# Optimization experiments

Hardware: AMD Instinct MI355X
Metric: run time of the kernel (lower is better)

Reference implementation:

```python
import jax, jax.numpy as jnp
import numpy as np

L = 48                 # lattice side
M = 2 * L * L          # 4608 spin-orbitals (spinful: 2 per site)
N_OCC = 1024           # occupied fermions
N_HID = 24             # hidden fermions
NT2 = 2 * N_HID        # pairing channels in CNN output
JASTROW = 16
CH = NT2 + JASTROW     # 64 CNN channels
NBLOCKS = 4
K = 3                  # conv kernel size


def conv2d_circular(x, w, b):
    # x: (C,H,W), w: (O,I,K,K); 'SAME' conv with circular (periodic) padding
    p = K // 2
    xp = jnp.pad(x, ((0, 0), (p, p), (p, p)), mode='wrap')
    y = jax.lax.conv_general_dilated(xp[None], w, (1, 1), 'VALID',
                                     dimension_numbers=('NCHW', 'OIHW', 'NCHW'))[0]
    if b is not None:
        y = y + b[:, None, None]
    return y


def cnn_forward(x, params):
    # ReshapeConv: flat spinful config (M,) -> (2, L, L)
    h = x.reshape(2, L, L)
    for i, (w1, b1, w2, b2) in enumerate(params):
        res = h
        t = h / jnp.sqrt(i + 1.0)
        t = t / jnp.sqrt(2.0) if i == 0 else jax.nn.gelu(t)
        t = jax.nn.gelu(conv2d_circular(t, w1, b1))
        t = conv2d_circular(t, w2, b2)
        if t.shape[0] > res.shape[0]:
            res = jnp.repeat(res, t.shape[0] // res.shape[0], axis=0)
        h = t + res
    return h / jnp.sqrt(NBLOCKS + 1.0)


def pfaffian_sign(A):
    # Sign of the Pfaffian of skew-symmetric A via Householder tridiagonalization.
    # pf(A) = det(Q) * prod(superdiag of T over even positions); det(Q)=(-1)^{#reflections}.
    n = A.shape[0]
    idx = jnp.arange(n)

    def body(k, carry):
        A, ds = carry
        col = A[:, k]
        xv = jnp.where(idx > k, col, 0.0)
        normx = jnp.sqrt(jnp.sum(xv * xv))
        s = jnp.where(col[k + 1] >= 0, 1.0, -1.0)
        v = xv - (-s * normx) * (idx == k + 1).astype(A.dtype)
        vn = jnp.sqrt(jnp.sum(v * v))
        ok = vn > 1e-30
        v = jnp.where(ok, v / jnp.where(ok, vn, 1.0), 0.0)
        u = A @ v
        # H A H for skew A with H = I - 2 v v^T  (v^T A v = 0)
        A = A + 2.0 * jnp.outer(v, u) - 2.0 * jnp.outer(u, v)
        return A, jnp.where(ok, -ds, ds)

    A, ds = jax.lax.fori_loop(0, n - 2, body, (A, jnp.array(1.0, A.dtype)))
    sup = jnp.diagonal(A, offset=1)[::2]
    return ds * jnp.prod(jnp.sign(sup))


def setup_inputs() -> dict:
    key = jax.random.key(0)
    ks = jax.random.split(key, 32)
    # occupation config in {+1,-1} with exactly N_OCC occupied modes
    occ = jnp.concatenate([jnp.ones(N_OCC, jnp.float32), -jnp.ones(M - N_OCC, jnp.float32)])
    x = jax.random.permutation(ks[0], occ)

    def he(k, shape):
        fan_in = shape[1] * shape[2] * shape[3]
        return jax.random.normal(k, shape, jnp.float32) * jnp.sqrt(2.0 / fan_in)

    inp = {
        'x': x,
        'F_vv': jax.random.normal(ks[1], (M, M), jnp.float32),
        'F_hh': jax.random.normal(ks[2], (N_HID, N_HID), jnp.float32),
    }
    j = 3
    for b in range(NBLOCKS):
        cin = 2 if b == 0 else CH
        inp[f'w1_{b}'] = he(ks[j], (CH, cin, K, K)); j += 1
        inp[f'b1_{b}'] = jnp.zeros((CH,), jnp.float32)
        inp[f'w2_{b}'] = he(ks[j], (CH, CH, K, K)); j += 1
        if b < NBLOCKS - 1:  # last block conv2 has no bias
            inp[f'b2_{b}'] = jnp.zeros((CH,), jnp.float32)
    return inp


def reference(x, F_vv, F_hh,
              w1_0, b1_0, w2_0, b2_0,
              w1_1, b1_1, w2_1, b2_1,
              w1_2, b1_2, w2_2, b2_2,
              w1_3, b1_3, w2_3):
    params = [(w1_0, b1_0, w2_0, b2_0),
              (w1_1, b1_1, w2_1, b2_1),
              (w1_2, b1_2, w2_2, b2_2),
              (w1_3, b1_3, w2_3, None)]
    out = cnn_forward(x, params)                     # (CH, L, L)
    n = jnp.nonzero(x == 1, size=N_OCC)[0]           # occupied mode indices
    log_J = out[NT2:].sum()                          # Jastrow log-factor (real)
    F_vh = out[:NT2].reshape(-1, M).T                # (M, N_HID)
    Fvv = 0.5 * (F_vv - F_vv.T)
    Fvh_n = F_vh[n]                                  # (N_OCC, N_HID)
    A = jnp.block([[Fvv[n][:, n], Fvh_n],
                   [-Fvh_n.T, 0.5 * (F_hh - F_hh.T)]])  # (N_OCC+N_HID,)^2 skew
    sign = pfaffian_sign(jax.lax.stop_gradient(A))   # cos(angle(sign)) == sign for real dtype
    logabspf = 0.5 * jnp.linalg.slogdet(A)[1]        # |pf(A)| = sqrt(|det(A)|)
    return sign, logabspf + log_J
```

## Files before the change

### kernel.cpp

```cpp
#include <hip/hip_runtime.h>
#include <math.h>


#define NPIX 2304
#define MSZ  4608
#define NOCC 1024
#define NHID 24
#define PF_N 1048

__device__ __forceinline__ float gelu_f(float v){
  float v3 = v*v*v;
  return 0.5f*v*(1.0f + tanhf(0.7978845608028654f*(v + 0.044715f*v3)));
}

__global__ void k_prep(const float* __restrict__ x, int* __restrict__ nidx,
                       float* __restrict__ tbuf){
  __shared__ int cnt[256];
  __shared__ int off[256];
  int t = threadIdx.x;
  int c = 0;
  for (int k = 0; k < 18; k++){
    int idx = t*18 + k;
    float v = x[idx];
    c += (v == 1.0f) ? 1 : 0;
    tbuf[idx] = v * 0.70710678118654752f;
  }
  cnt[t] = c;
  __syncthreads();
  if (t == 0){ int s = 0; for (int q=0;q<256;q++){ off[q]=s; s+=cnt[q]; } }
  __syncthreads();
  int o = off[t];
  for (int k = 0; k < 18; k++){
    int idx = t*18+k;
    if (x[idx] == 1.0f) nidx[o++] = idx;
  }
}

__global__ __launch_bounds__(128) void k_conv(const float* __restrict__ in,
      const float* __restrict__ wgt, const float* __restrict__ bias,
      const float* __restrict__ res, float* __restrict__ outp,
      float* __restrict__ pre_out, double* __restrict__ logJ_acc,
      int cin, int resmode, int dogelu, float scale, float pre_scale){
  const int c  = blockIdx.x / 6;
  const int rg = blockIdx.x % 6;
  const int tid = threadIdx.x;
  const int y  = rg*8 + (tid >> 4);
  const int xg = (tid & 15)*3;
  const int ym = ((y+47)%48)*48, y0 = y*48, yp = ((y+1)%48)*48;
  int c5[5];
  #pragma unroll
  for (int t = 0; t < 5; t++){
    int xx = xg - 1 + t;
    c5[t] = (xx < 0) ? 47 : ((xx >= 48) ? xx - 48 : xx);
  }
  float s0 = 0.f, s1 = 0.f, s2 = 0.f;
  const float* wp = wgt + c*cin*9;
  for (int ci = 0; ci < cin; ci++){
    const float* b_ = in + ci*NPIX;
    #pragma unroll
    for (int rr = 0; rr < 3; rr++){
      const int rb = (rr == 0) ? ym : ((rr == 1) ? y0 : yp);
      float v0 = b_[rb+c5[0]], v1 = b_[rb+c5[1]], v2 = b_[rb+c5[2]];
      float v3 = b_[rb+c5[3]], v4 = b_[rb+c5[4]];
      float w0 = wp[3*rr], w1 = wp[3*rr+1], w2 = wp[3*rr+2];
      s0 += v0*w0 + v1*w1 + v2*w2;
      s1 += v1*w0 + v2*w1 + v3*w2;
      s2 += v2*w0 + v3*w1 + v4*w2;
    }
    wp += 9;
  }
  const float bv = bias ? bias[c] : 0.f;
  const int base = c*NPIX + y0 + xg;
  float sv[3] = {s0, s1, s2};
  double ls = 0.0;
  #pragma unroll
  for (int t = 0; t < 3; t++){
    float s = sv[t] + bv;
    if (dogelu) s = gelu_f(s);
    if (resmode == 1) s += res[c*NPIX + y0 + xg + t];
    else if (resmode == 2) s += res[(c>>5)*NPIX + y0 + xg + t];
    s *= scale;
    outp[base+t] = s;
    if (pre_out) pre_out[base+t] = gelu_f(s * pre_scale);
    ls += (double)s;
  }
  if (logJ_acc && c >= 48){
    for (int o = 32; o > 0; o >>= 1) ls += __shfl_down(ls, o, 64);
    if ((tid & 63) == 0) atomicAdd(logJ_acc, ls);
  }
}

__global__ __launch_bounds__(256) void k_buildAvv(const float* __restrict__ Fvv,
      const int* __restrict__ nidx, double* __restrict__ A){
  __shared__ float G1[32][33], G2[32][33];
  __shared__ int sNi[32], sNj[32];
  int I = 0, item = blockIdx.x;
  while ((I+1)*(I+2)/2 <= item) I++;
  const int J = item - I*(I+1)/2;
  const int i0 = I*32, j0 = J*32;
  const int tid = threadIdx.x;
  if (tid < 32){ sNi[tid] = nidx[i0+tid]; }
  else if (tid < 64){ sNj[tid-32] = nidx[j0+tid-32]; }
  __syncthreads();
  for (int idx = tid; idx < 32*32; idx += 256){
    const int r = idx >> 5, c = idx & 31;
    G1[r][c] = Fvv[(size_t)sNi[r]*MSZ + sNj[c]];
    G2[r][c] = Fvv[(size_t)sNj[r]*MSZ + sNi[c]];
  }
  __syncthreads();
  for (int idx = tid; idx < 32*32; idx += 256){
    const int r = idx >> 5, c = idx & 31;
    const int i = i0 + r, j = j0 + c;
    if (i > j)
      A[(size_t)i*PF_N + j] = 0.5*((double)G1[r][c] - (double)G2[c][r]);
  }
}

__global__ void k_buildAs(const float* __restrict__ Fhh,
      const float* __restrict__ hfin, const int* __restrict__ nidx,
      double* __restrict__ A){
  int g = blockIdx.x*256 + threadIdx.x;
  if (g >= 24*PF_N) return;
  const int i = NOCC + g / PF_N, j = g % PF_N;
  if (j >= i) return;
  const int r = i - NOCC;
  double v;
  if (j < NOCC){
    int nj = nidx[j];
    int ss = (nj >= NPIX) ? 1 : 0;
    v = -(double)hfin[(2*r+ss)*NPIX + (nj - ss*NPIX)];
  } else {
    int r2 = j - NOCC;
    v = 0.5*((double)Fhh[r*NHID + r2] - (double)Fhh[r2*NHID + r]);
  }
  A[(size_t)i*PF_N + j] = v;
}

__device__ __forceinline__ void factor_lds(double* D, double* sTf, int w,
      double* __restrict__ histN, double& lv_out, int& sg_out){
  const int tid = threadIdx.x;
  const int r = tid & 63, qu = tid >> 6;
  const int np = w >> 1;
  for (int j = 0; j < np; j++){
    const int r0 = 2*j, r1 = r0 + 1;
    const double t = -D[r1*65 + r0];
    const double invt = 1.0 / t;
    if (tid == 0) sTf[j] = t;
    const bool rowok = (r < w) && (r >= r0 + 2);
    if (rowok){
      const double ar = D[r*65 + r0], br = D[r*65 + r1];
      if (qu == 0){
        histN[32 + j*64 + r]        = ar * invt;
        histN[32 + 2048 + j*64 + r] = br * invt;
      }
      const int lo = r0 + 2, hi = r;
      const int per = (hi - lo + 3) >> 2;
      const int cb = lo + qu*per;
      int ce = cb + per; if (ce > hi) ce = hi;
      for (int c = cb; c < ce; c++){
        const double ac = D[c*65 + r0], bc = D[c*65 + r1];
        D[r*65 + c] += (br*ac - ar*bc) * invt;
      }
    }
    __syncthreads();
  }
  if (tid < np) histN[tid] = 1.0 / sTf[tid];
  lv_out = 0.0; sg_out = 0;
  if (tid < 64){
    double lv = 0.0; int sg = 0;
    if (tid < np){ double t = sTf[tid]; lv = log(fabs(t)); sg = (t < 0.0) ? 1 : 0; }
    for (int o = 32; o > 0; o >>= 1){
      lv += __shfl_down(lv, o, 64);
      sg += __shfl_down(sg, o, 64);
    }
    if (tid == 0){ lv_out = lv; sg_out = sg; }
  }
}

__global__ __launch_bounds__(256) void k_panelD0(const double* __restrict__ A,
      double* __restrict__ hist, double* __restrict__ lacc,
      int* __restrict__ nneg){
  __shared__ double D[64*65];
  __shared__ double sTf[32];
  const int tid = threadIdx.x;
  for (int idx = tid; idx < 64*64; idx += 256){
    int r = idx >> 6, c = idx & 63;
    if (r > c) D[r*65+c] = A[(size_t)r*PF_N + c];
  }
  __syncthreads();
  double lv; int sg;
  factor_lds(D, sTf, 64, hist, lv, sg);
  if (tid == 0){ atomicAdd(lacc, lv); atomicAdd(nneg, sg); }
}

__global__ __launch_bounds__(256) void k_panelR(double* __restrict__ A,
      const double* __restrict__ hist, int k){
  const int N = PF_N, c0 = 64*k, tc0 = c0 + 64;
  const int wv = threadIdx.x >> 6, lc = threadIdx.x & 63;
  const int i = tc0 + blockIdx.x*4 + wv;
  if (i >= N) return;
  double v = A[(size_t)i*N + c0 + lc];
  const double* hA = hist + 32;
  const double* hB = hist + 32 + 2048;
  #pragma unroll 8
  for (int j = 0; j < 32; j++){
    double a = __shfl(v, 2*j,   64);
    double b = __shfl(v, 2*j+1, 64);
    if (lc >= 2*j+2) v += b*hA[j*64+lc] - a*hB[j*64+lc];
  }
  A[(size_t)i*N + c0 + lc] = v;
}

__global__ __launch_bounds__(256) void k_trail(double* __restrict__ A,
      const double* __restrict__ histR, double* __restrict__ histW,
      double* __restrict__ lacc, int* __restrict__ nneg,
      const double* __restrict__ logJ, float* __restrict__ outp,
      int k, int fin){
  const int N = PF_N, c0 = 64*k, tc0 = c0 + 64;
  const int tid = threadIdx.x;
  int I = 0, item = blockIdx.x;
  while ((I+1)*(I+2)/2 <= item) I++;
  const int J = item - I*(I+1)/2;
  const int i0 = tc0 + I*64, j0 = tc0 + J*64;
  const int iend = (i0 + 64 < N) ? (i0 + 64) : N;
  const int jend = (j0 + 64 < N) ? (j0 + 64) : N;
  __shared__ double shmem[4224];
  __shared__ double sInvL[32];
  __shared__ double sTf[32];
  double* sPiA = shmem;
  double* sPiB = shmem + 1056;
  double* sPjA = shmem + 2112;
  double* sPjB = shmem + 3168;
  if (tid < 32) sInvL[tid] = histR[tid];
  const int ty = tid >> 4, tx = tid & 15;
  double acc[4][4];
  #pragma unroll
  for (int rr = 0; rr < 4; rr++)
    #pragma unroll
    for (int cc = 0; cc < 4; cc++){
      const int i = i0 + ty + 16*rr, j = j0 + tx + 16*cc;
      acc[rr][cc] = (i < iend && j < jend && i > j) ? A[(size_t)i*N + j] : 0.0;
    }
  __syncthreads();
  #pragma unroll
  for (int lh = 0; lh < 2; lh++){
    #pragma unroll
    for (int u = 0; u < 4; u++){
      const int idx = tid + u*256;
      const int r = idx >> 4, ll = idx & 15;
      const int l = lh*16 + ll;
      const double it = sInvL[l];
      const int gi = i0 + r;
      double a = 0.0, b = 0.0;
      if (gi < iend){
        a = A[(size_t)gi*N + c0 + 2*l];
        b = A[(size_t)gi*N + c0 + 2*l + 1];
      }
      sPiA[ll*66+r] = a; sPiB[ll*66+r] = b;
      const int gj = j0 + r;
      double a2 = 0.0, b2 = 0.0;
      if (gj < jend){
        a2 = A[(size_t)gj*N + c0 + 2*l];
        b2 = A[(size_t)gj*N + c0 + 2*l + 1];
      }
      sPjA[ll*66+r] = a2*it; sPjB[ll*66+r] = b2*it;
    }
    __syncthreads();
    #pragma unroll 4
    for (int ll = 0; ll < 16; ll++){
      double ar[4], br[4], ac[4], bc[4];
      #pragma unroll
      for (int rr = 0; rr < 4; rr++){
        ar[rr] = sPiA[ll*66 + ty + 16*rr];
        br[rr] = sPiB[ll*66 + ty + 16*rr];
      }
      #pragma unroll
      for (int cc = 0; cc < 4; cc++){
        ac[cc] = sPjA[ll*66 + tx + 16*cc];
        bc[cc] = sPjB[ll*66 + tx + 16*cc];
      }
      #pragma unroll
      for (int rr = 0; rr < 4; rr++)
        #pragma unroll
        for (int cc = 0; cc < 4; cc++)
          acc[rr][cc] += br[rr]*ac[cc] - ar[rr]*bc[cc];
    }
    __syncthreads();
  }
  #pragma unroll
  for (int rr = 0; rr < 4; rr++)
    #pragma unroll
    for (int cc = 0; cc < 4; cc++){
      const int i = i0 + ty + 16*rr, j = j0 + tx + 16*cc;
      if (i < iend && j < jend && i > j) A[(size_t)i*N + j] = acc[rr][cc];
    }
  if (blockIdx.x == 0){
    __syncthreads();
    const int wn = iend - i0;
    #pragma unroll
    for (int rr = 0; rr < 4; rr++)
      #pragma unroll
      for (int cc = 0; cc < 4; cc++){
        const int i = i0 + ty + 16*rr, j = j0 + tx + 16*cc;
        if (i < iend && j < jend && i > j)
          shmem[(i - i0)*65 + (j - j0)] = acc[rr][cc];
      }
    __syncthreads();
    double lv; int sg;
    factor_lds(shmem, sTf, wn, histW, lv, sg);
    if (tid == 0){
      double lold = atomicAdd(lacc, lv);
      int sold = atomicAdd(nneg, sg);
      if (fin){
        int stot = sold + sg;
        outp[0] = (stot & 1) ? -1.0f : 1.0f;
        outp[1] = (float)(lold + lv + logJ[0]);
      }
    }
  }
}

extern "C" void kernel_launch(void* const* d_in, const int* in_sizes, int n_in,
                              void* d_out, int out_size, void* d_ws, size_t ws_size,
                              hipStream_t stream){
  (void)in_sizes; (void)n_in; (void)out_size; (void)ws_size;
  const float* x   = (const float*)d_in[0];
  const float* Fvv = (const float*)d_in[1];
  const float* Fhh = (const float*)d_in[2];
  const float* w1[4] = {(const float*)d_in[3], (const float*)d_in[7],
                        (const float*)d_in[11], (const float*)d_in[15]};
  const float* b1[4] = {(const float*)d_in[4], (const float*)d_in[8],
                        (const float*)d_in[12], (const float*)d_in[16]};
  const float* w2[4] = {(const float*)d_in[5], (const float*)d_in[9],
                        (const float*)d_in[13], (const float*)d_in[17]};
  const float* b2[3] = {(const float*)d_in[6], (const float*)d_in[10],
                        (const float*)d_in[14]};

  char* ws = (char*)d_ws;
  double* lacc  = (double*)(ws + 0);
  int*    nneg  = (int*)(ws + 8);
  double* logJa = (double*)(ws + 1024);
  int*    nidx  = (int*)(ws + 1088);
  double* hist0 = (double*)(ws + 8192);
  double* hist1 = (double*)(ws + 41216);
  const size_t CB = 589824;
  float* tbuf  = (float*)(ws + 74240);
  float* ybuf  = (float*)(ws + 74240 + CB);
  float* hbuf0 = (float*)(ws + 74240 + 2*CB);
  float* hbuf1 = (float*)(ws + 74240 + 3*CB);
  double* A    = (double*)(ws + 74240 + 4*CB);

  hipMemsetAsync(d_ws, 0, 2048, stream);
  k_prep<<<1,256,0,stream>>>(x, nidx, tbuf);

  k_conv<<<384,128,0,stream>>>(tbuf, w1[0], b1[0], nullptr, ybuf,
                               nullptr, nullptr, 2, 0, 1, 1.0f, 0.f);
  k_conv<<<384,128,0,stream>>>(ybuf, w2[0], b2[0], x, hbuf0,
                               tbuf, nullptr, 64, 2, 0, 1.0f,
                               0.70710678118654752f);
  k_conv<<<384,128,0,stream>>>(tbuf, w1[1], b1[1], nullptr, ybuf,
                               nullptr, nullptr, 64, 0, 1, 1.0f, 0.f);
  k_conv<<<384,128,0,stream>>>(ybuf, w2[1], b2[1], hbuf0, hbuf1,
                               tbuf, nullptr, 64, 1, 0, 1.0f,
                               0.57735026918962576f);
  k_conv<<<384,128,0,stream>>>(tbuf, w1[2], b1[2], nullptr, ybuf,
                               nullptr, nullptr, 64, 0, 1, 1.0f, 0.f);
  k_conv<<<384,128,0,stream>>>(ybuf, w2[2], b2[2], hbuf1, hbuf0,
                               tbuf, nullptr, 64, 1, 0, 1.0f, 0.5f);
  k_conv<<<384,128,0,stream>>>(tbuf, w1[3], b1[3], nullptr, ybuf,
                               nullptr, nullptr, 64, 0, 1, 1.0f, 0.f);
  k_conv<<<384,128,0,stream>>>(ybuf, w2[3], nullptr, hbuf0, hbuf1,
                               nullptr, logJa, 64, 1, 0,
                               0.44721359549995794f, 0.f);

  k_buildAvv<<<528,256,0,stream>>>(Fvv, nidx, A);
  k_buildAs<<<(24*PF_N+255)/256,256,0,stream>>>(Fhh, hbuf1, nidx, A);

  k_panelD0<<<1,256,0,stream>>>(A, hist0, lacc, nneg);
  for (int k = 0; k < 16; k++){
    double* hR = (k & 1) ? hist1 : hist0;
    double* hW = (k & 1) ? hist0 : hist1;
    const int m = PF_N - 64*(k+1);
    k_panelR<<<(m+3)/4,256,0,stream>>>(A, hR, k);
    const int nt = (m + 63) >> 6;
    k_trail<<<nt*(nt+1)/2,256,0,stream>>>(A, hR, hW, lacc, nneg, logJa,
                                          (float*)d_out, k, (k == 15) ? 1 : 0);
  }
}
```

Before: 1.119 ms.

## Fuse whole pipeline into one cooperative persistent kernel with grid syncs

Replaces the separate prep, conv, A-build, panel and trailing-update launches with a single cooperative kernel. Stages are separated by grid-wide barriers. Fvv gather tiles and the first panel factorization now run on spare blocks while the conv layers execute. This removes per-launch overhead and idle gaps between the roughly forty small kernels. In exchange, every stage is capped at 256 resident blocks, and each grid.sync adds its own barrier cost.

```diff
diff --git a/kernel.cpp b/kernel.cpp
--- a/kernel.cpp
+++ b/kernel.cpp
@@ -1,5 +1,8 @@
 #include <hip/hip_runtime.h>
+#include <hip/hip_cooperative_groups.h>
 #include <math.h>
+
+namespace cg = cooperative_groups;
 
 
 #define NPIX 2304
@@ -13,37 +16,14 @@
   return 0.5f*v*(1.0f + tanhf(0.7978845608028654f*(v + 0.044715f*v3)));
 }
 
-__global__ void k_prep(const float* __restrict__ x, int* __restrict__ nidx,
-                       float* __restrict__ tbuf){
-  __shared__ int cnt[256];
-  __shared__ int off[256];
-  int t = threadIdx.x;
-  int c = 0;
-  for (int k = 0; k < 18; k++){
-    int idx = t*18 + k;
-    float v = x[idx];
-    c += (v == 1.0f) ? 1 : 0;
-    tbuf[idx] = v * 0.70710678118654752f;
-  }
-  cnt[t] = c;
-  __syncthreads();
-  if (t == 0){ int s = 0; for (int q=0;q<256;q++){ off[q]=s; s+=cnt[q]; } }
-  __syncthreads();
-  int o = off[t];
-  for (int k = 0; k < 18; k++){
-    int idx = t*18+k;
-    if (x[idx] == 1.0f) nidx[o++] = idx;
-  }
-}
-
-__global__ __launch_bounds__(128) void k_conv(const float* __restrict__ in,
-      const float* __restrict__ wgt, const float* __restrict__ bias,
-      const float* __restrict__ res, float* __restrict__ outp,
-      float* __restrict__ pre_out, double* __restrict__ logJ_acc,
-      int cin, int resmode, int dogelu, float scale, float pre_scale){
-  const int c  = blockIdx.x / 6;
-  const int rg = blockIdx.x % 6;
-  const int tid = threadIdx.x;
+__device__ __forceinline__ void conv_unit(int u, int tid,
+    const float* __restrict__ in, const float* __restrict__ wgt,
+    const float* __restrict__ bias, const float* __restrict__ res,
+    float* __restrict__ outp, float* __restrict__ pre_out,
+    double* __restrict__ logJ_acc,
+    int cin, int resmode, int dogelu, float scale, float pre_scale){
+  const int c  = u / 6;
+  const int rg = u % 6;
   const int y  = rg*8 + (tid >> 4);
   const int xg = (tid & 15)*3;
   const int ym = ((y+47)%48)*48, y0 = y*48, yp = ((y+1)%48)*48;
@@ -90,50 +70,30 @@
   }
 }
 
-__global__ __launch_bounds__(256) void k_buildAvv(const float* __restrict__ Fvv,
-      const int* __restrict__ nidx, double* __restrict__ A){
-  __shared__ float G1[32][33], G2[32][33];
-  __shared__ int sNi[32], sNj[32];
-  int I = 0, item = blockIdx.x;
+__device__ void build_avv_tile(int item, const float* __restrict__ Fvv,
+      const int* __restrict__ nidx, double* __restrict__ A,
+      float* G1, float* G2, int* sNi, int* sNj){
+  __syncthreads();
+  int I = 0;
   while ((I+1)*(I+2)/2 <= item) I++;
   const int J = item - I*(I+1)/2;
   const int i0 = I*32, j0 = J*32;
   const int tid = threadIdx.x;
-  if (tid < 32){ sNi[tid] = nidx[i0+tid]; }
-  else if (tid < 64){ sNj[tid-32] = nidx[j0+tid-32]; }
+  if (tid < 32) sNi[tid] = nidx[i0+tid];
+  else if (tid < 64) sNj[tid-32] = nidx[j0+tid-32];
   __syncthreads();
   for (int idx = tid; idx < 32*32; idx += 256){
     const int r = idx >> 5, c = idx & 31;
-    G1[r][c] = Fvv[(size_t)sNi[r]*MSZ + sNj[c]];
-    G2[r][c] = Fvv[(size_t)sNj[r]*MSZ + sNi[c]];
+    G1[r*33+c] = Fvv[(size_t)sNi[r]*MSZ + sNj[c]];
+    G2[r*33+c] = Fvv[(size_t)sNj[r]*MSZ + sNi[c]];
   }
   __syncthreads();
   for (int idx = tid; idx < 32*32; idx += 256){
     const int r = idx >> 5, c = idx & 31;
     const int i = i0 + r, j = j0 + c;
     if (i > j)
-      A[(size_t)i*PF_N + j] = 0.5*((double)G1[r][c] - (double)G2[c][r]);
-  }
-}
-
-__global__ void k_buildAs(const float* __restrict__ Fhh,
-      const float* __restrict__ hfin, const int* __restrict__ nidx,
-      double* __restrict__ A){
-  int g = blockIdx.x*256 + threadIdx.x;
-  if (g >= 24*PF_N) return;
-  const int i = NOCC + g / PF_N, j = g % PF_N;
-  if (j >= i) return;
-  const int r = i - NOCC;
-  double v;
-  if (j < NOCC){
-    int nj = nidx[j];
-    int ss = (nj >= NPIX) ? 1 : 0;
-    v = -(double)hfin[(2*r+ss)*NPIX + (nj - ss*NPIX)];
-  } else {
-    int r2 = j - NOCC;
-    v = 0.5*((double)Fhh[r*NHID + r2] - (double)Fhh[r2*NHID + r]);
-  }
-  A[(size_t)i*PF_N + j] = v;
+      A[(size_t)i*PF_N + j] = 0.5*((double)G1[r*33+c] - (double)G2[c*33+r]);
+  }
 }
 
 __device__ __forceinline__ void factor_lds(double* D, double* sTf, int w,
@@ -177,145 +137,242 @@
   }
 }
 
-__global__ __launch_bounds__(256) void k_panelD0(const double* __restrict__ A,
-      double* __restrict__ hist, double* __restrict__ lacc,
-      int* __restrict__ nneg){
-  __shared__ double D[64*65];
-  __shared__ double sTf[32];
-  const int tid = threadIdx.x;
-  for (int idx = tid; idx < 64*64; idx += 256){
-    int r = idx >> 6, c = idx & 63;
-    if (r > c) D[r*65+c] = A[(size_t)r*PF_N + c];
-  }
-  __syncthreads();
-  double lv; int sg;
-  factor_lds(D, sTf, 64, hist, lv, sg);
-  if (tid == 0){ atomicAdd(lacc, lv); atomicAdd(nneg, sg); }
-}
-
-__global__ __launch_bounds__(256) void k_panelR(double* __restrict__ A,
-      const double* __restrict__ hist, int k){
-  const int N = PF_N, c0 = 64*k, tc0 = c0 + 64;
-  const int wv = threadIdx.x >> 6, lc = threadIdx.x & 63;
-  const int i = tc0 + blockIdx.x*4 + wv;
-  if (i >= N) return;
-  double v = A[(size_t)i*N + c0 + lc];
-  const double* hA = hist + 32;
-  const double* hB = hist + 32 + 2048;
-  #pragma unroll 8
-  for (int j = 0; j < 32; j++){
-    double a = __shfl(v, 2*j,   64);
-    double b = __shfl(v, 2*j+1, 64);
-    if (lc >= 2*j+2) v += b*hA[j*64+lc] - a*hB[j*64+lc];
-  }
-  A[(size_t)i*N + c0 + lc] = v;
-}
-
-__global__ __launch_bounds__(256) void k_trail(double* __restrict__ A,
-      const double* __restrict__ histR, double* __restrict__ histW,
-      double* __restrict__ lacc, int* __restrict__ nneg,
-      const double* __restrict__ logJ, float* __restrict__ outp,
-      int k, int fin){
-  const int N = PF_N, c0 = 64*k, tc0 = c0 + 64;
-  const int tid = threadIdx.x;
-  int I = 0, item = blockIdx.x;
-  while ((I+1)*(I+2)/2 <= item) I++;
-  const int J = item - I*(I+1)/2;
-  const int i0 = tc0 + I*64, j0 = tc0 + J*64;
-  const int iend = (i0 + 64 < N) ? (i0 + 64) : N;
-  const int jend = (j0 + 64 < N) ? (j0 + 64) : N;
-  __shared__ double shmem[4224];
+__global__ __launch_bounds__(256) void k_mega(
+    const float* __restrict__ x, const float* __restrict__ Fvv,
+    const float* __restrict__ Fhh,
+    const float* __restrict__ w10, const float* __restrict__ b10,
+    const float* __restrict__ w20, const float* __restrict__ b20,
+    const float* __restrict__ w11, const float* __restrict__ b11,
+    const float* __restrict__ w21, const float* __restrict__ b21,
+    const float* __restrict__ w12, const float* __restrict__ b12,
+    const float* __restrict__ w22, const float* __restrict__ b22,
+    const float* __restrict__ w13, const float* __restrict__ b13,
+    const float* __restrict__ w23,
+    float* __restrict__ outp,
+    double* __restrict__ lacc, int* __restrict__ nneg,
+    double* __restrict__ logJa, int* __restrict__ nidx,
+    double* __restrict__ hist0, double* __restrict__ hist1,
+    float* __restrict__ tbuf, float* __restrict__ ybuf,
+    float* __restrict__ hbuf0, float* __restrict__ hbuf1,
+    double* __restrict__ A){
+  cg::grid_group grid = cg::this_grid();
+  const int bid = blockIdx.x, tid = threadIdx.x;
+  __shared__ double shU[4224];
   __shared__ double sInvL[32];
   __shared__ double sTf[32];
-  double* sPiA = shmem;
-  double* sPiB = shmem + 1056;
-  double* sPjA = shmem + 2112;
-  double* sPjB = shmem + 3168;
-  if (tid < 32) sInvL[tid] = histR[tid];
-  const int ty = tid >> 4, tx = tid & 15;
-  double acc[4][4];
+
+  if (bid == 0){
+    int* cnt = (int*)shU; int* off = cnt + 256;
+    if (tid == 0){ *lacc = 0.0; *nneg = 0; *logJa = 0.0; }
+    int c = 0;
+    for (int k2 = 0; k2 < 18; k2++){
+      int idx = tid*18 + k2;
+      float v = x[idx];
+      c += (v == 1.0f) ? 1 : 0;
+      tbuf[idx] = v * 0.70710678118654752f;
+    }
+    cnt[tid] = c;
+    __syncthreads();
+    if (tid == 0){ int s = 0; for (int q=0;q<256;q++){ off[q]=s; s+=cnt[q]; } }
+    __syncthreads();
+    int o = off[tid];
+    for (int k2 = 0; k2 < 18; k2++){
+      int idx = tid*18+k2;
+      if (x[idx] == 1.0f) nidx[o++] = idx;
+    }
+  }
+  grid.sync();
+
+  const float* cin_p[8] = {tbuf,ybuf,tbuf,ybuf,tbuf,ybuf,tbuf,ybuf};
+  const float* w_p[8]   = {w10,w20,w11,w21,w12,w22,w13,w23};
+  const float* b_p[8]   = {b10,b20,b11,b21,b12,b22,b13,nullptr};
+  const float* r_p[8]   = {nullptr,x,nullptr,hbuf0,nullptr,hbuf1,nullptr,hbuf0};
+  float* o_p[8]         = {ybuf,hbuf0,ybuf,hbuf1,ybuf,hbuf0,ybuf,hbuf1};
+  float* pre_p[8]       = {nullptr,tbuf,nullptr,tbuf,nullptr,tbuf,nullptr,nullptr};
+  const int   cinn[8]   = {2,64,64,64,64,64,64,64};
+  const int   rm[8]     = {0,2,0,1,0,1,0,1};
+  const int   dg[8]     = {1,0,1,0,1,0,1,0};
+  const float sc[8]     = {1.f,1.f,1.f,1.f,1.f,1.f,1.f,0.44721359549995794f};
+  const float ps[8]     = {0.f,0.70710678118654752f,0.f,0.57735026918962576f,
+                           0.f,0.5f,0.f,0.f};
   #pragma unroll
-  for (int rr = 0; rr < 4; rr++)
-    #pragma unroll
-    for (int cc = 0; cc < 4; cc++){
-      const int i = i0 + ty + 16*rr, j = j0 + tx + 16*cc;
-      acc[rr][cc] = (i < iend && j < jend && i > j) ? A[(size_t)i*N + j] : 0.0;
-    }
-  __syncthreads();
-  #pragma unroll
-  for (int lh = 0; lh < 2; lh++){
-    #pragma unroll
-    for (int u = 0; u < 4; u++){
-      const int idx = tid + u*256;
-      const int r = idx >> 4, ll = idx & 15;
-      const int l = lh*16 + ll;
-      const double it = sInvL[l];
-      const int gi = i0 + r;
-      double a = 0.0, b = 0.0;
-      if (gi < iend){
-        a = A[(size_t)gi*N + c0 + 2*l];
-        b = A[(size_t)gi*N + c0 + 2*l + 1];
-      }
-      sPiA[ll*66+r] = a; sPiB[ll*66+r] = b;
-      const int gj = j0 + r;
-      double a2 = 0.0, b2 = 0.0;
-      if (gj < jend){
-        a2 = A[(size_t)gj*N + c0 + 2*l];
-        b2 = A[(size_t)gj*N + c0 + 2*l + 1];
-      }
-      sPjA[ll*66+r] = a2*it; sPjB[ll*66+r] = b2*it;
-    }
-    __syncthreads();
-    #pragma unroll 4
-    for (int ll = 0; ll < 16; ll++){
-      double ar[4], br[4], ac[4], bc[4];
-      #pragma unroll
-      for (int rr = 0; rr < 4; rr++){
-        ar[rr] = sPiA[ll*66 + ty + 16*rr];
-        br[rr] = sPiB[ll*66 + ty + 16*rr];
-      }
-      #pragma unroll
-      for (int cc = 0; cc < 4; cc++){
-        ac[cc] = sPjA[ll*66 + tx + 16*cc];
-        bc[cc] = sPjB[ll*66 + tx + 16*cc];
-      }
-      #pragma unroll
-      for (int rr = 0; rr < 4; rr++)
+  for (int p = 1; p <= 8; p++){
+    if (bid < 192){
+      conv_unit(bid*2 + (tid>>7), tid & 127,
+                cin_p[p-1], w_p[p-1], b_p[p-1], r_p[p-1], o_p[p-1], pre_p[p-1],
+                (p == 8) ? logJa : nullptr,
+                cinn[p-1], rm[p-1], dg[p-1], sc[p-1], ps[p-1]);
+    } else if (bid < 255){
+      float* G1 = (float*)shU;
+      float* G2 = G1 + 32*33;
+      int* sNi = (int*)(G2 + 32*33);
+      int* sNj = sNi + 32;
+      for (int t = (p-1)*66 + (bid-192); t < p*66; t += 63)
+        build_avv_tile(t, Fvv, nidx, A, G1, G2, sNi, sNj);
+    } else if (p == 2){
+      for (int idx = tid; idx < 64*64; idx += 256){
+        int r = idx >> 6, c = idx & 63;
+        if (r > c) shU[r*65+c] = A[(size_t)r*PF_N + c];
+      }
+      __syncthreads();
+      double lv; int sg;
+      factor_lds(shU, sTf, 64, hist0, lv, sg);
+      if (tid == 0){ atomicAdd(lacc, lv); atomicAdd(nneg, sg); }
+    }
+    grid.sync();
+  }
+
+  {
+    int g0 = bid*256 + tid;
+    if (g0 < 24*PF_N){
+      const int i = NOCC + g0 / PF_N, j = g0 % PF_N;
+      if (j < i){
+        const int r = i - NOCC;
+        double v;
+        if (j < NOCC){
+          int nj = nidx[j];
+          int ss = (nj >= NPIX) ? 1 : 0;
+          v = -(double)hbuf1[(2*r+ss)*NPIX + (nj - ss*NPIX)];
+        } else {
+          int r2 = j - NOCC;
+          v = 0.5*((double)Fhh[r*NHID + r2] - (double)Fhh[r2*NHID + r]);
+        }
+        A[(size_t)i*PF_N + j] = v;
+      }
+    }
+  }
+  grid.sync();
+
+  for (int k = 0; k < 16; k++){
+    const double* hR = (k & 1) ? hist1 : hist0;
+    double* hW = (k & 1) ? hist0 : hist1;
+    const int N = PF_N, c0 = 64*k, tc0 = c0 + 64;
+
+    {
+      const int wv = tid >> 6, lc = tid & 63;
+      const int i = tc0 + bid*4 + wv;
+      if (i < N){
+        double v = A[(size_t)i*N + c0 + lc];
+        const double* hA = hR + 32;
+        const double* hB = hR + 32 + 2048;
+        #pragma unroll 8
+        for (int j = 0; j < 32; j++){
+          double a = __shfl(v, 2*j,   64);
+          double b = __shfl(v, 2*j+1, 64);
+          if (lc >= 2*j+2) v += b*hA[j*64+lc] - a*hB[j*64+lc];
+        }
+        A[(size_t)i*N + c0 + lc] = v;
+      }
+    }
+    grid.sync();
+
+    {
+      const int m = N - tc0;
+      const int nt = (m + 63) >> 6;
+      const int items = nt*(nt+1)/2;
+      double* sPiA = shU;
+      double* sPiB = shU + 1056;
+      double* sPjA = shU + 2112;
+      double* sPjB = shU + 3168;
+      const int ty = tid >> 4, tx = tid & 15;
+      int i0 = tc0, j0 = tc0, iend = tc0, jend = tc0;
+      double acc[4][4];
+      if (bid < items){
+        {
+          int I = 0, item = bid;
+          while ((I+1)*(I+2)/2 <= item) I++;
+          const int J = item - I*(I+1)/2;
+          i0 = tc0 + I*64; j0 = tc0 + J*64;
+        }
+        iend = (i0 + 64 < N) ? (i0 + 64) : N;
+        jend = (j0 + 64 < N) ? (j0 + 64) : N;
+        if (tid < 32) sInvL[tid] = hR[tid];
         #pragma unroll
-        for (int cc = 0; cc < 4; cc++)
-          acc[rr][cc] += br[rr]*ac[cc] - ar[rr]*bc[cc];
-    }
-    __syncthreads();
-  }
-  #pragma unroll
-  for (int rr = 0; rr < 4; rr++)
-    #pragma unroll
-    for (int cc = 0; cc < 4; cc++){
-      const int i = i0 + ty + 16*rr, j = j0 + tx + 16*cc;
-      if (i < iend && j < jend && i > j) A[(size_t)i*N + j] = acc[rr][cc];
-    }
-  if (blockIdx.x == 0){
-    __syncthreads();
-    const int wn = iend - i0;
-    #pragma unroll
-    for (int rr = 0; rr < 4; rr++)
-      #pragma unroll
-      for (int cc = 0; cc < 4; cc++){
-        const int i = i0 + ty + 16*rr, j = j0 + tx + 16*cc;
-        if (i < iend && j < jend && i > j)
-          shmem[(i - i0)*65 + (j - j0)] = acc[rr][cc];
-      }
-    __syncthreads();
-    double lv; int sg;
-    factor_lds(shmem, sTf, wn, histW, lv, sg);
-    if (tid == 0){
-      double lold = atomicAdd(lacc, lv);
-      int sold = atomicAdd(nneg, sg);
-      if (fin){
-        int stot = sold + sg;
-        outp[0] = (stot & 1) ? -1.0f : 1.0f;
-        outp[1] = (float)(lold + lv + logJ[0]);
-      }
+        for (int rr = 0; rr < 4; rr++)
+          #pragma unroll
+          for (int cc = 0; cc < 4; cc++){
+            const int i = i0 + ty + 16*rr, j = j0 + tx + 16*cc;
+            acc[rr][cc] = (i < iend && j < jend && i > j) ? A[(size_t)i*N + j] : 0.0;
+          }
+        __syncthreads();
+        #pragma unroll
+        for (int lh = 0; lh < 2; lh++){
+          #pragma unroll
+          for (int u2 = 0; u2 < 4; u2++){
+            const int idx = tid + u2*256;
+            const int r = idx >> 4, ll = idx & 15;
+            const int l = lh*16 + ll;
+            const double it = sInvL[l];
+            const int gi = i0 + r;
+            double a = 0.0, b = 0.0;
+            if (gi < iend){
+              a = A[(size_t)gi*N + c0 + 2*l];
+              b = A[(size_t)gi*N + c0 + 2*l + 1];
+            }
+            sPiA[ll*66+r] = a; sPiB[ll*66+r] = b;
+            const int gj = j0 + r;
+            double a2 = 0.0, b2 = 0.0;
+            if (gj < jend){
+              a2 = A[(size_t)gj*N + c0 + 2*l];
+              b2 = A[(size_t)gj*N + c0 + 2*l + 1];
+            }
+            sPjA[ll*66+r] = a2*it; sPjB[ll*66+r] = b2*it;
+          }
+          __syncthreads();
+          #pragma unroll 4
+          for (int ll = 0; ll < 16; ll++){
+            double ar[4], br[4], ac2[4], bc2[4];
+            #pragma unroll
+            for (int rr = 0; rr < 4; rr++){
+              ar[rr] = sPiA[ll*66 + ty + 16*rr];
+              br[rr] = sPiB[ll*66 + ty + 16*rr];
+            }
+            #pragma unroll
+            for (int cc = 0; cc < 4; cc++){
+              ac2[cc] = sPjA[ll*66 + tx + 16*cc];
+              bc2[cc] = sPjB[ll*66 + tx + 16*cc];
+            }
+            #pragma unroll
+            for (int rr = 0; rr < 4; rr++)
+              #pragma unroll
+              for (int cc = 0; cc < 4; cc++)
+                acc[rr][cc] += br[rr]*ac2[cc] - ar[rr]*bc2[cc];
+          }
+          __syncthreads();
+        }
+        #pragma unroll
+        for (int rr = 0; rr < 4; rr++)
+          #pragma unroll
+          for (int cc = 0; cc < 4; cc++){
+            const int i = i0 + ty + 16*rr, j = j0 + tx + 16*cc;
+            if (i < iend && j < jend && i > j) A[(size_t)i*N + j] = acc[rr][cc];
+          }
+      }
+      if (bid == 0){
+        __syncthreads();
+        const int wn = iend - i0;
+        #pragma unroll
+        for (int rr = 0; rr < 4; rr++)
+          #pragma unroll
+          for (int cc = 0; cc < 4; cc++){
+            const int i = i0 + ty + 16*rr, j = j0 + tx + 16*cc;
+            if (i < iend && j < jend && i > j)
+              shU[(i - i0)*65 + (j - j0)] = acc[rr][cc];
+          }
+        __syncthreads();
+        double lv; int sg;
+        factor_lds(shU, sTf, wn, hW, lv, sg);
+        if (tid == 0){
+          double lold = atomicAdd(lacc, lv);
+          int sold = atomicAdd(nneg, sg);
+          if (k == 15){
+            int stot = sold + sg;
+            outp[0] = (stot & 1) ? -1.0f : 1.0f;
+            outp[1] = (float)(lold + lv + logJa[0]);
+          }
+        }
+      }
+      grid.sync();
     }
   }
 }
@@ -327,14 +384,22 @@
   const float* x   = (const float*)d_in[0];
   const float* Fvv = (const float*)d_in[1];
   const float* Fhh = (const float*)d_in[2];
-  const float* w1[4] = {(const float*)d_in[3], (const float*)d_in[7],
-                        (const float*)d_in[11], (const float*)d_in[15]};
-  const float* b1[4] = {(const float*)d_in[4], (const float*)d_in[8],
-                        (const float*)d_in[12], (const float*)d_in[16]};
-  const float* w2[4] = {(const float*)d_in[5], (const float*)d_in[9],
-                        (const float*)d_in[13], (const float*)d_in[17]};
-  const float* b2[3] = {(const float*)d_in[6], (const float*)d_in[10],
-                        (const float*)d_in[14]};
+  const float* w10 = (const float*)d_in[3];
+  const float* b10 = (const float*)d_in[4];
+  const float* w20 = (const float*)d_in[5];
+  const float* b20 = (const float*)d_in[6];
+  const float* w11 = (const float*)d_in[7];
+  const float* b11 = (const float*)d_in[8];
+  const float* w21 = (const float*)d_in[9];
+  const float* b21 = (const float*)d_in[10];
+  const float* w12 = (const float*)d_in[11];
+  const float* b12 = (const float*)d_in[12];
+  const float* w22 = (const float*)d_in[13];
+  const float* b22 = (const float*)d_in[14];
+  const float* w13 = (const float*)d_in[15];
+  const float* b13 = (const float*)d_in[16];
+  const float* w23 = (const float*)d_in[17];
+  float* outp = (float*)d_out;
 
   char* ws = (char*)d_ws;
   double* lacc  = (double*)(ws + 0);
@@ -350,40 +415,9 @@
   float* hbuf1 = (float*)(ws + 74240 + 3*CB);
   double* A    = (double*)(ws + 74240 + 4*CB);
 
-  hipMemsetAsync(d_ws, 0, 2048, stream);
-  k_prep<<<1,256,0,stream>>>(x, nidx, tbuf);
-
-  k_conv<<<384,128,0,stream>>>(tbuf, w1[0], b1[0], nullptr, ybuf,
-                               nullptr, nullptr, 2, 0, 1, 1.0f, 0.f);
-  k_conv<<<384,128,0,stream>>>(ybuf, w2[0], b2[0], x, hbuf0,
-                               tbuf, nullptr, 64, 2, 0, 1.0f,
-                               0.70710678118654752f);
-  k_conv<<<384,128,0,stream>>>(tbuf, w1[1], b1[1], nullptr, ybuf,
-                               nullptr, nullptr, 64, 0, 1, 1.0f, 0.f);
-  k_conv<<<384,128,0,stream>>>(ybuf, w2[1], b2[1], hbuf0, hbuf1,
-                               tbuf, nullptr, 64, 1, 0, 1.0f,
-                               0.57735026918962576f);
-  k_conv<<<384,128,0,stream>>>(tbuf, w1[2], b1[2], nullptr, ybuf,
-                               nullptr, nullptr, 64, 0, 1, 1.0f, 0.f);
-  k_conv<<<384,128,0,stream>>>(ybuf, w2[2], b2[2], hbuf1, hbuf0,
-                               tbuf, nullptr, 64, 1, 0, 1.0f, 0.5f);
-  k_conv<<<384,128,0,stream>>>(tbuf, w1[3], b1[3], nullptr, ybuf,
-                               nullptr, nullptr, 64, 0, 1, 1.0f, 0.f);
-  k_conv<<<384,128,0,stream>>>(ybuf, w2[3], nullptr, hbuf0, hbuf1,
-                               nullptr, logJa, 64, 1, 0,
-                               0.44721359549995794f, 0.f);
-
-  k_buildAvv<<<528,256,0,stream>>>(Fvv, nidx, A);
-  k_buildAs<<<(24*PF_N+255)/256,256,0,stream>>>(Fhh, hbuf1, nidx, A);
-
-  k_panelD0<<<1,256,0,stream>>>(A, hist0, lacc, nneg);
-  for (int k = 0; k < 16; k++){
-    double* hR = (k & 1) ? hist1 : hist0;
-    double* hW = (k & 1) ? hist0 : hist1;
-    const int m = PF_N - 64*(k+1);
-    k_panelR<<<(m+3)/4,256,0,stream>>>(A, hR, k);
-    const int nt = (m + 63) >> 6;
-    k_trail<<<nt*(nt+1)/2,256,0,stream>>>(A, hR, hW, lacc, nneg, logJa,
-                                          (float*)d_out, k, (k == 15) ? 1 : 0);
-  }
-}
+  void* args[] = { &x,&Fvv,&Fhh,&w10,&b10,&w20,&b20,&w11,&b11,&w21,&b21,
+                   &w12,&b12,&w22,&b22,&w13,&b13,&w23,&outp,
+                   &lacc,&nneg,&logJa,&nidx,&hist0,&hist1,
+                   &tbuf,&ybuf,&hbuf0,&hbuf1,&A };
+  hipLaunchCooperativeKernel((void*)k_mega, dim3(256), dim3(256), args, 0, stream);
+}
```

After: 2.075 ms. +85.5%, slower.
